# Optimization experiments

Measured on AMD Instinct MI355X. Metric: run time of the kernel, lower is better.

## Reference

```python
import jax, jax.numpy as jnp
import numpy as np

NB = 4          # bits per symbol (QAM16)
K = 3           # num_streams
M = 8           # rx antennas
B = 4096        # batch
NPTS = 2 ** NB  # constellation points per stream
C = NPTS ** K   # exhaustive candidate vectors


def _pam_gray(b):
    if len(b) > 1:
        return (1 - 2 * b[0]) * (2 ** len(b[1:]) - _pam_gray(b[1:]))
    return 1 - 2 * b[0]


def _qam_points(nb):
    # Gray-labeled QAM, normalized to unit average energy (as sionna's Constellation)
    n = 2 ** nb
    pts = np.zeros(n, np.complex64)
    for i in range(n):
        b = np.array(list(np.binary_repr(i, nb)), int)
        pts[i] = _pam_gray(b[0::2]) + 1j * _pam_gray(b[1::2])
    pts /= np.sqrt(np.mean(np.abs(pts) ** 2)).astype(np.float32)
    return pts.astype(np.complex64)


def _candidates():
    pts = _qam_points(NB)
    idx = np.arange(C)
    # per-stream symbol indices, stream 0 is most significant (vec_list order)
    sym_idx = np.stack([(idx // NPTS ** (K - 1 - k)) % NPTS for k in range(K)], axis=1)  # [C,K]
    xc = pts[sym_idx]  # [C,K] complex candidate symbol vectors
    # bits: MSB-first per symbol -> [C, K, NB]
    bits = ((sym_idx[..., None] >> (NB - 1 - np.arange(NB))) & 1).astype(bool)
    return xc, bits.reshape(C, K * NB)


_XC, _BITS = _candidates()


def setup_inputs() -> dict:
    key = jax.random.key(0)
    ks = jax.random.split(key, 6)
    y_re = jax.random.normal(ks[0], (B, M), jnp.float32)
    y_im = jax.random.normal(ks[1], (B, M), jnp.float32)
    h_re = jax.random.normal(ks[2], (B, M, K), jnp.float32)
    h_im = jax.random.normal(ks[3], (B, M, K), jnp.float32)
    # Hermitian PD noise covariance S = F F^H / M + 2 I
    fr = jax.random.normal(ks[4], (B, M, M), jnp.float32)
    fi = jax.random.normal(ks[5], (B, M, M), jnp.float32)
    F = fr + 1j * fi
    S = jnp.einsum('bij,bkj->bik', F, F.conj()) / M + 2.0 * jnp.eye(M, dtype=jnp.complex64)
    return {"y_re": y_re, "y_im": y_im, "h_re": h_re, "h_im": h_im,
            "s_re": jnp.real(S), "s_im": jnp.imag(S)}


def reference(y_re, y_im, h_re, h_im, s_re, s_im):
    y = y_re + 1j * y_im            # [B,M]
    h = h_re + 1j * h_im            # [B,M,K]
    s = s_re + 1j * s_im            # [B,M,M] Hermitian PD
    # Whiten: L L^H = S ; ||L^{-1}(y - Hx)||^2 = (y-Hx)^H S^{-1} (y-Hx)
    L = jnp.linalg.cholesky(s)
    yw = jax.scipy.linalg.solve_triangular(L, y[..., None], lower=True)[..., 0]  # [B,M]
    hw = jax.scipy.linalg.solve_triangular(L, h, lower=True)                     # [B,M,K]

    xc = jnp.asarray(_XC)                         # [C,K]
    G = jnp.einsum('bmk,bml->bkl', hw.conj(), hw)  # [B,K,K] Gram
    z = jnp.einsum('bm,bmk->bk', yw.conj(), hw)    # [B,K]  y~^H H~
    P = xc.conj()[:, :, None] * xc[:, None, :]     # [C,K,K] candidate outer products
    quad = jnp.real(jnp.einsum('bkl,ckl->bc', G, P))   # x^H G x
    cross = jnp.real(jnp.einsum('bk,ck->bc', z, xc))   # Re(y~^H H~ x)
    yn = jnp.sum(jnp.abs(yw) ** 2, axis=-1, keepdims=True)
    d = yn - 2.0 * cross + quad                   # [B,C] exhaustive squared distances

    # maxlog bit LLRs: LLR = min_{bit=0} d - min_{bit=1} d
    bits = jnp.asarray(_BITS)                     # [C, K*NB] bool
    BIG = jnp.float32(1e30)
    llrs = []
    for p in range(K * NB):  # fixed small loop over bit positions
        mask = bits[:, p]
        min1 = jnp.min(jnp.where(mask, d, BIG), axis=1)
        min0 = jnp.min(jnp.where(mask, BIG, d), axis=1)
        llrs.append(min0 - min1)
    return jnp.stack(llrs, axis=-1).reshape(B, K, NB)
```

## Files before the change

kernel.cpp:

```cpp
#include <hip/hip_runtime.h>
#include <math.h>

#define BIG 1e30f

__device__ __forceinline__ constexpr float QR(int i) {
    return ((((i >> 3) & 1) ? -1.0f : 1.0f) * ((((i >> 1) & 1) ? 3.0f : 1.0f)) *
            0.31622776601683794f);
}
__device__ __forceinline__ constexpr float QI(int i) {
    return ((((i >> 2) & 1) ? -1.0f : 1.0f) * (((i & 1) ? 3.0f : 1.0f)) *
            0.31622776601683794f);
}

__global__ __launch_bounds__(256, 1) void mld_fused(
    const float* __restrict__ y_re, const float* __restrict__ y_im,
    const float* __restrict__ h_re, const float* __restrict__ h_im,
    const float* __restrict__ s_re, const float* __restrict__ s_im,
    float* __restrict__ out) {
    int b = blockIdx.x;
    int tid = threadIdx.x;

    __shared__ float s_xr[4][8], s_xi[4][8];
    __shared__ float s_w[16];
    __shared__ float s_tmin[256];
    __shared__ float s_r[32];
    __shared__ float s_m2[32];

    if (tid < 64) {
        int ii = tid >> 3, kk = tid & 7;
        float ar = s_re[b * 64 + tid];
        float ai = s_im[b * 64 + tid];
        float br = 0.0f, bi = 0.0f;
        if (kk == 0) {
            br = y_re[b * 8 + ii];
            bi = y_im[b * 8 + ii];
        } else if (kk < 4) {
            br = h_re[b * 24 + ii * 3 + (kk - 1)];
            bi = h_im[b * 24 + ii * 3 + (kk - 1)];
        }

#pragma unroll
        for (int j = 0; j < 8; ++j) {
            float djr = __shfl(ar, j * 9, 64);
            float dinv = 1.0f / sqrtf(djr);
            if (kk == j && ii >= j) { ar *= dinv; ai *= dinv; }
            float Lijr = __shfl(ar, ii * 8 + j, 64), Liji = __shfl(ai, ii * 8 + j, 64);
            float Lkjr = __shfl(ar, kk * 8 + j, 64), Lkji = __shfl(ai, kk * 8 + j, 64);
            if (kk > j && ii >= kk) {
                ar -= Lijr * Lkjr + Liji * Lkji;
                ai -= Liji * Lkjr - Lijr * Lkji;
            }
        }

#pragma unroll
        for (int k = 0; k < 8; ++k) {
            float dk = __shfl(ar, k * 9, 64);
            float dinvk = 1.0f / dk;
            if (ii == k) { br *= dinvk; bi *= dinvk; }
            float xkr = __shfl(br, k * 8 + kk, 64), xki = __shfl(bi, k * 8 + kk, 64);
            float Likr = __shfl(ar, ii * 8 + k, 64), Liki = __shfl(ai, ii * 8 + k, 64);
            if (ii > k) {
                br -= Likr * xkr - Liki * xki;
                bi -= Likr * xki + Liki * xkr;
            }
        }
        if (kk < 4) { s_xr[kk][ii] = br; s_xi[kk][ii] = bi; }
    }
    __syncthreads();

    if (tid < 9) {
        int a = (int)((0x000211321ull >> (tid * 4)) & 15ull);
        int c = (int)((0x321332321ull >> (tid * 4)) & 15ull);
        float sr = 0.0f, si = 0.0f;
#pragma unroll
        for (int m = 0; m < 8; ++m) {
            float xar = s_xr[a][m], xai = s_xi[a][m];
            float xbr = s_xr[c][m], xbi = s_xi[c][m];
            sr += xar * xbr + xai * xbi;
            si += xar * xbi - xai * xbr;
        }
        if (tid < 3) {
            s_w[tid] = sr;
        } else {
            int base = 3 + (tid - 3) * 2;
            s_w[base] = sr;
            s_w[base + 1] = si;
        }
    }
    __syncthreads();

    float g00 = s_w[0], g11 = s_w[1], g22 = s_w[2];
    float g01r = s_w[3], g01i = s_w[4], g02r = s_w[5], g02i = s_w[6];
    float g12r = s_w[7], g12i = s_w[8];
    float z0r = s_w[9], z0i = s_w[10], z1r = s_w[11], z1i = s_w[12];
    float z2r = s_w[13], z2i = s_w[14];

    int i0 = tid >> 4, i1 = tid & 15;
    float p0r = QR(i0), p0i = QI(i0);
    float p1r = QR(i1), p1i = QI(i1);
    float n0 = p0r * p0r + p0i * p0i;
    float n1 = p1r * p1r + p1i * p1i;

    float a0 = g00 * n0 - 2.0f * (z0r * p0r - z0i * p0i);
    float a1 = g11 * n1 - 2.0f * (z1r * p1r - z1i * p1i);
    float crr = p0r * p1r + p0i * p1i;
    float cri = p0r * p1i - p0i * p1r;
    float base = a0 + a1 + 2.0f * (g01r * crr - g01i * cri);
    float w0r = g02r * p0r + g02i * p0i;
    float w0i = g02i * p0r - g02r * p0i;
    float w1r = g12r * p1r + g12i * p1i;
    float w1i = g12i * p1r - g12r * p1i;
    float cr = 2.0f * (w0r + w1r - z2r);
    float ci = -2.0f * (w0i + w1i - z2i);

    float m2[8];
#pragma unroll
    for (int j = 0; j < 8; ++j) m2[j] = BIG;
#pragma unroll
    for (int i2 = 0; i2 < 16; ++i2) {
        float pr = QR(i2), pi = QI(i2);
        float d = base + g22 * (pr * pr + pi * pi) + cr * pr + ci * pi;
        m2[0 + ((i2 >> 3) & 1)] = fminf(m2[0 + ((i2 >> 3) & 1)], d);
        m2[2 + ((i2 >> 2) & 1)] = fminf(m2[2 + ((i2 >> 2) & 1)], d);
        m2[4 + ((i2 >> 1) & 1)] = fminf(m2[4 + ((i2 >> 1) & 1)], d);
        m2[6 + (i2 & 1)]        = fminf(m2[6 + (i2 & 1)], d);
    }
    float tmin = fminf(m2[0], m2[1]);

    s_tmin[tid] = tmin;

#pragma unroll
    for (int j = 0; j < 8; ++j) {
        float v = m2[j];
#pragma unroll
        for (int mask = 1; mask < 64; mask <<= 1) v = fminf(v, __shfl_xor(v, mask, 64));
        m2[j] = v;
    }
    int wave = tid >> 6, lane = tid & 63;
    if (lane == 0) {
#pragma unroll
        for (int j = 0; j < 8; ++j) s_m2[wave * 8 + j] = m2[j];
    }
    __syncthreads();

    if (tid < 16) {
        float m = BIG;
#pragma unroll
        for (int j = 0; j < 16; ++j) m = fminf(m, s_tmin[tid * 16 + j]);
        s_r[tid] = m;
    } else if (tid < 32) {
        int i1x = tid - 16;
        float m = BIG;
#pragma unroll
        for (int j = 0; j < 16; ++j) m = fminf(m, s_tmin[j * 16 + i1x]);
        s_r[16 + i1x] = m;
    }
    __syncthreads();

    if (tid < 12) {
        int k = tid >> 2, n = tid & 3, sh = 3 - n;
        float m0 = BIG, m1 = BIG;
        if (k < 2) {
            const float* r = s_r + k * 16;
#pragma unroll
            for (int j = 0; j < 16; ++j) {
                float v = r[j];
                if ((j >> sh) & 1) m1 = fminf(m1, v);
                else m0 = fminf(m0, v);
            }
        } else {
#pragma unroll
            for (int wv = 0; wv < 4; ++wv) {
                m0 = fminf(m0, s_m2[wv * 8 + n * 2 + 0]);
                m1 = fminf(m1, s_m2[wv * 8 + n * 2 + 1]);
            }
        }
        out[b * 12 + tid] = m0 - m1;
    }
}

extern "C" void kernel_launch(void* const* d_in, const int* in_sizes, int n_in,
                              void* d_out, int out_size, void* d_ws, size_t ws_size,
                              hipStream_t stream) {
    const float* y_re = (const float*)d_in[0];
    const float* y_im = (const float*)d_in[1];
    const float* h_re = (const float*)d_in[2];
    const float* h_im = (const float*)d_in[3];
    const float* s_re = (const float*)d_in[4];
    const float* s_im = (const float*)d_in[5];
    int B = in_sizes[0] / 8;

    mld_fused<<<dim3(B), dim3(256), 0, stream>>>(y_re, y_im, h_re, h_im, s_re, s_im,
                                                 (float*)d_out);
}
```

Baseline: 82.10 us.

## Map one batch item per wavefront and reduce LLRs with wave shuffles

Restructures the kernel so each 64-lane wavefront handles one batch element, with four elements per block, instead of one block per element. Before, only one wave did the Cholesky solve while three sat idle. Each lane now loops over four stream-0 symbols that share a magnitude class and folds the stream-2 energy into three precomputed bases. Most block-level shared-memory reductions become in-wave shuffle reductions, and the launch-bounds occupancy limit of one block is dropped. The catch is more registers per lane and a longer serial inner loop.

```diff
diff --git a/kernel.cpp b/kernel.cpp
--- a/kernel.cpp
+++ b/kernel.cpp
@@ -2,34 +2,34 @@
 #include <math.h>
 
 #define BIG 1e30f
+#define RT10 0.31622776601683794f
 
 __device__ __forceinline__ constexpr float QR(int i) {
-    return ((((i >> 3) & 1) ? -1.0f : 1.0f) * ((((i >> 1) & 1) ? 3.0f : 1.0f)) *
-            0.31622776601683794f);
+    return ((((i >> 3) & 1) ? -1.0f : 1.0f) * ((((i >> 1) & 1) ? 3.0f : 1.0f)) * RT10);
 }
 __device__ __forceinline__ constexpr float QI(int i) {
-    return ((((i >> 2) & 1) ? -1.0f : 1.0f) * (((i & 1) ? 3.0f : 1.0f)) *
-            0.31622776601683794f);
-}
-
-__global__ __launch_bounds__(256, 1) void mld_fused(
+    return ((((i >> 2) & 1) ? -1.0f : 1.0f) * (((i & 1) ? 3.0f : 1.0f)) * RT10);
+}
+
+__global__ __launch_bounds__(256) void mld_wave(
     const float* __restrict__ y_re, const float* __restrict__ y_im,
     const float* __restrict__ h_re, const float* __restrict__ h_im,
     const float* __restrict__ s_re, const float* __restrict__ s_im,
-    float* __restrict__ out) {
-    int b = blockIdx.x;
+    float* __restrict__ out, int B) {
     int tid = threadIdx.x;
-
-    __shared__ float s_xr[4][8], s_xi[4][8];
-    __shared__ float s_w[16];
-    __shared__ float s_tmin[256];
-    __shared__ float s_r[32];
-    __shared__ float s_m2[32];
-
-    if (tid < 64) {
-        int ii = tid >> 3, kk = tid & 7;
-        float ar = s_re[b * 64 + tid];
-        float ai = s_im[b * 64 + tid];
+    int w = tid >> 6, lane = tid & 63;
+    int b = blockIdx.x * 4 + w;
+    bool live = (b < B);
+    if (!live) b = B - 1;
+
+    __shared__ float s_xr[4][4][8], s_xi[4][4][8];
+    __shared__ float s_w[4][16];
+    __shared__ float s16[4][16];
+
+    {
+        int ii = lane >> 3, kk = lane & 7;
+        float ar = s_re[b * 64 + lane];
+        float ai = s_im[b * 64 + lane];
         float br = 0.0f, bi = 0.0f;
         if (kk == 0) {
             br = y_re[b * 8 + ii];
@@ -51,7 +51,6 @@
                 ai -= Liji * Lkjr - Lijr * Lkji;
             }
         }
-
 #pragma unroll
         for (int k = 0; k < 8; ++k) {
             float dk = __shfl(ar, k * 9, 64);
@@ -64,118 +63,130 @@
                 bi -= Likr * xki + Liki * xkr;
             }
         }
-        if (kk < 4) { s_xr[kk][ii] = br; s_xi[kk][ii] = bi; }
+        if (kk < 4) { s_xr[w][kk][ii] = br; s_xi[w][kk][ii] = bi; }
     }
     __syncthreads();
 
-    if (tid < 9) {
-        int a = (int)((0x000211321ull >> (tid * 4)) & 15ull);
-        int c = (int)((0x321332321ull >> (tid * 4)) & 15ull);
+    if (lane < 9) {
+        int pa = (int)((0x000211321ull >> (lane * 4)) & 15ull);
+        int pc = (int)((0x321332321ull >> (lane * 4)) & 15ull);
         float sr = 0.0f, si = 0.0f;
 #pragma unroll
         for (int m = 0; m < 8; ++m) {
-            float xar = s_xr[a][m], xai = s_xi[a][m];
-            float xbr = s_xr[c][m], xbi = s_xi[c][m];
+            float xar = s_xr[w][pa][m], xai = s_xi[w][pa][m];
+            float xbr = s_xr[w][pc][m], xbi = s_xi[w][pc][m];
             sr += xar * xbr + xai * xbi;
             si += xar * xbi - xai * xbr;
         }
-        if (tid < 3) {
-            s_w[tid] = sr;
+        if (lane < 3) {
+            s_w[w][lane] = sr;
         } else {
-            int base = 3 + (tid - 3) * 2;
-            s_w[base] = sr;
-            s_w[base + 1] = si;
+            int base2 = 3 + (lane - 3) * 2;
+            s_w[w][base2] = sr;
+            s_w[w][base2 + 1] = si;
         }
     }
     __syncthreads();
 
-    float g00 = s_w[0], g11 = s_w[1], g22 = s_w[2];
-    float g01r = s_w[3], g01i = s_w[4], g02r = s_w[5], g02i = s_w[6];
-    float g12r = s_w[7], g12i = s_w[8];
-    float z0r = s_w[9], z0i = s_w[10], z1r = s_w[11], z1i = s_w[12];
-    float z2r = s_w[13], z2i = s_w[14];
-
-    int i0 = tid >> 4, i1 = tid & 15;
-    float p0r = QR(i0), p0i = QI(i0);
+    const float* ww = s_w[w];
+    float g00 = ww[0], g11 = ww[1], g22 = ww[2];
+    float g01r = ww[3], g01i = ww[4], g02r = ww[5], g02i = ww[6];
+    float g12r = ww[7], g12i = ww[8];
+    float z0r = ww[9], z0i = ww[10], z1r = ww[11], z1i = ww[12];
+    float z2r = ww[13], z2i = ww[14];
+
+    int a = lane >> 4, i1 = lane & 15;
     float p1r = QR(i1), p1i = QI(i1);
-    float n0 = p0r * p0r + p0i * p0i;
     float n1 = p1r * p1r + p1i * p1i;
-
-    float a0 = g00 * n0 - 2.0f * (z0r * p0r - z0i * p0i);
-    float a1 = g11 * n1 - 2.0f * (z1r * p1r - z1i * p1i);
-    float crr = p0r * p1r + p0i * p1i;
-    float cri = p0r * p1i - p0i * p1r;
-    float base = a0 + a1 + 2.0f * (g01r * crr - g01i * cri);
-    float w0r = g02r * p0r + g02i * p0i;
-    float w0i = g02i * p0r - g02r * p0i;
+    float a1c = g11 * n1 - 2.0f * (z1r * p1r - z1i * p1i);
     float w1r = g12r * p1r + g12i * p1i;
     float w1i = g12i * p1r - g12r * p1i;
-    float cr = 2.0f * (w0r + w1r - z2r);
-    float ci = -2.0f * (w0i + w1i - z2i);
-
-    float m2[8];
-#pragma unroll
-    for (int j = 0; j < 8; ++j) m2[j] = BIG;
-#pragma unroll
-    for (int i2 = 0; i2 < 16; ++i2) {
-        float pr = QR(i2), pi = QI(i2);
-        float d = base + g22 * (pr * pr + pi * pi) + cr * pr + ci * pi;
-        m2[0 + ((i2 >> 3) & 1)] = fminf(m2[0 + ((i2 >> 3) & 1)], d);
-        m2[2 + ((i2 >> 2) & 1)] = fminf(m2[2 + ((i2 >> 2) & 1)], d);
-        m2[4 + ((i2 >> 1) & 1)] = fminf(m2[4 + ((i2 >> 1) & 1)], d);
-        m2[6 + (i2 & 1)]        = fminf(m2[6 + (i2 & 1)], d);
-    }
-    float tmin = fminf(m2[0], m2[1]);
-
-    s_tmin[tid] = tmin;
-
-#pragma unroll
-    for (int j = 0; j < 8; ++j) {
-        float v = m2[j];
+    float mr0 = (a & 2) ? 3.0f * RT10 : RT10;
+    float mi0 = (a & 1) ? 3.0f * RT10 : RT10;
+    float n0 = mr0 * mr0 + mi0 * mi0;
+    float g00n0 = g00 * n0;
+
+    float ch[12];
+#pragma unroll
+    for (int j = 0; j < 12; ++j) ch[j] = BIG;
+    float u[4];
+#pragma unroll
+    for (int q = 0; q < 4; ++q) {
+        float p0r = (q & 2) ? -mr0 : mr0;
+        float p0i = (q & 1) ? -mi0 : mi0;
+        float a0c = g00n0 - 2.0f * (z0r * p0r - z0i * p0i);
+        float crr = p0r * p1r + p0i * p1i;
+        float cri = p0r * p1i - p0i * p1r;
+        float base = a0c + a1c + 2.0f * (g01r * crr - g01i * cri);
+        float w0r = g02r * p0r + g02i * p0i;
+        float w0i = g02i * p0r - g02r * p0i;
+        float cr = 2.0f * (w0r + w1r - z2r);
+        float ci = -2.0f * (w0i + w1i - z2i);
+        float bA = fmaf(g22, 0.2f, base);
+        float bB = fmaf(g22, 1.0f, base);
+        float bC = fmaf(g22, 1.8f, base);
+        float pmin = BIG;
+#pragma unroll
+        for (int i2 = 0; i2 < 16; ++i2) {
+            int cls = ((i2 >> 1) & 1) + (i2 & 1);
+            float bX = (cls == 0) ? bA : (cls == 1 ? bB : bC);
+            float d = fmaf(QI(i2), ci, fmaf(QR(i2), cr, bX));
+            pmin = fminf(pmin, d);
+            ch[0 + ((i2 >> 3) & 1)] = fminf(ch[0 + ((i2 >> 3) & 1)], d);
+            ch[2 + ((i2 >> 2) & 1)] = fminf(ch[2 + ((i2 >> 2) & 1)], d);
+            ch[4 + ((i2 >> 1) & 1)] = fminf(ch[4 + ((i2 >> 1) & 1)], d);
+            ch[6 + (i2 & 1)]        = fminf(ch[6 + (i2 & 1)], d);
+        }
+        u[q] = pmin;
+    }
+    ch[8] = fminf(u[0], u[1]);
+    ch[9] = fminf(u[2], u[3]);
+    ch[10] = fminf(u[0], u[2]);
+    ch[11] = fminf(u[1], u[3]);
+
+#pragma unroll
+    for (int j = 0; j < 12; ++j) {
+        float v = ch[j];
 #pragma unroll
         for (int mask = 1; mask < 64; mask <<= 1) v = fminf(v, __shfl_xor(v, mask, 64));
-        m2[j] = v;
-    }
-    int wave = tid >> 6, lane = tid & 63;
-    if (lane == 0) {
-#pragma unroll
-        for (int j = 0; j < 8; ++j) s_m2[wave * 8 + j] = m2[j];
-    }
+        ch[j] = v;
+    }
+
+    float t1 = fminf(fminf(u[0], u[1]), fminf(u[2], u[3]));
+    float r0 = t1;
+#pragma unroll
+    for (int mask = 1; mask <= 8; mask <<= 1) r0 = fminf(r0, __shfl_xor(r0, mask, 64));
+    float r1 = fminf(t1, __shfl_xor(t1, 16, 64));
+    r1 = fminf(r1, __shfl_xor(r1, 32, 64));
+    if (lane < 16) s16[w][lane] = r1;
+
+    float zv = fminf(r0, __shfl_xor(r0, 16, 64));
+    float llr2 = zv - __shfl_xor(zv, 32, 64);
+    float yv = fminf(r0, __shfl_xor(r0, 32, 64));
+    float llr3 = yv - __shfl_xor(yv, 16, 64);
     __syncthreads();
 
-    if (tid < 16) {
-        float m = BIG;
-#pragma unroll
-        for (int j = 0; j < 16; ++j) m = fminf(m, s_tmin[tid * 16 + j]);
-        s_r[tid] = m;
-    } else if (tid < 32) {
-        int i1x = tid - 16;
-        float m = BIG;
-#pragma unroll
-        for (int j = 0; j < 16; ++j) m = fminf(m, s_tmin[j * 16 + i1x]);
-        s_r[16 + i1x] = m;
-    }
-    __syncthreads();
-
-    if (tid < 12) {
-        int k = tid >> 2, n = tid & 3, sh = 3 - n;
-        float m0 = BIG, m1 = BIG;
-        if (k < 2) {
-            const float* r = s_r + k * 16;
+    if (live) {
+        float* ob = out + b * 12;
+        if (lane == 0) {
+            ob[0] = ch[8] - ch[9];
+            ob[1] = ch[10] - ch[11];
+            ob[2] = llr2;
+            ob[3] = llr3;
+        } else if (lane >= 4 && lane < 8) {
+            int k = 3 - (lane - 4);
+            float m0 = BIG, m1 = BIG;
 #pragma unroll
             for (int j = 0; j < 16; ++j) {
-                float v = r[j];
-                if ((j >> sh) & 1) m1 = fminf(m1, v);
+                float v = s16[w][j];
+                if ((j >> k) & 1) m1 = fminf(m1, v);
                 else m0 = fminf(m0, v);
             }
-        } else {
-#pragma unroll
-            for (int wv = 0; wv < 4; ++wv) {
-                m0 = fminf(m0, s_m2[wv * 8 + n * 2 + 0]);
-                m1 = fminf(m1, s_m2[wv * 8 + n * 2 + 1]);
-            }
-        }
-        out[b * 12 + tid] = m0 - m1;
+            ob[lane] = m0 - m1;
+        } else if (lane >= 8 && lane < 12) {
+            int n = lane - 8;
+            ob[lane] = ch[n * 2] - ch[n * 2 + 1];
+        }
     }
 }
 
@@ -190,6 +201,6 @@
     const float* s_im = (const float*)d_in[5];
     int B = in_sizes[0] / 8;
 
-    mld_fused<<<dim3(B), dim3(256), 0, stream>>>(y_re, y_im, h_re, h_im, s_re, s_im,
-                                                 (float*)d_out);
-}
+    mld_wave<<<dim3((B + 3) / 4), dim3(256), 0, stream>>>(y_re, y_im, h_re, h_im,
+                                                          s_re, s_im, (float*)d_out, B);
+}
```

Result: faster. 77.13 us (-6.1%).
